# Kernel optimization log

Measured on AMD Instinct MI355X. Metric: run time of the kernel, lower is better.

Reference implementation:

```python
import jax, jax.numpy as jnp
import numpy as np

N = 4096          # num_nodes == batch (every node sampled once)
D_EMB = 512       # n_embd (temporal encoder width)
D_GNN = 256       # gnn_embd
H = 2             # num_heads (hardcoded in GraphAttentionLayer default)
D_HEAD = D_GNN // H
FUS = D_EMB + D_GNN
EDGE_P = 32.0 / N # avg degree ~ max_neighbors
ALPHA = 0.2
NEG_INF = -9e15


def layer_norm(x, g, b, eps=1e-5):
    m = jnp.mean(x, axis=-1, keepdims=True)
    v = jnp.var(x, axis=-1, keepdims=True)
    return (x - m) / jnp.sqrt(v + eps) * g + b


def setup_inputs() -> dict:
    key = jax.random.key(0)
    ks = jax.random.split(key, 12)
    s = lambda fan: 1.0 / np.sqrt(fan)
    h_temporal = jax.random.normal(ks[0], (N, D_EMB), jnp.float32)
    node_indices = jnp.arange(N, dtype=jnp.int32)
    adj = (jax.random.uniform(ks[1], (N, N)) < EDGE_P).astype(jnp.float32)
    adj = jnp.maximum(adj, jnp.eye(N, dtype=jnp.float32))  # self-loops
    W_proj = jax.random.normal(ks[2], (D_EMB, D_GNN), jnp.float32) * s(D_EMB)
    b_proj = jnp.zeros((D_GNN,), jnp.float32)
    W_gat = jax.random.normal(ks[3], (H, D_GNN, D_HEAD), jnp.float32) * s(D_GNN)
    a_gat = jax.random.normal(ks[4], (H, 2 * D_HEAD), jnp.float32) * s(2 * D_HEAD)
    node_emb = jax.random.normal(ks[5], (N, D_GNN), jnp.float32) * 0.02
    ln_g = jnp.ones((D_GNN,), jnp.float32)
    ln_b = jnp.zeros((D_GNN,), jnp.float32)
    ln2_g = jnp.ones((FUS,), jnp.float32)
    ln2_b = jnp.zeros((FUS,), jnp.float32)
    W1 = jax.random.normal(ks[6], (FUS, FUS // 2), jnp.float32) * s(FUS)
    b1 = jnp.zeros((FUS // 2,), jnp.float32)
    W2 = jax.random.normal(ks[7], (FUS // 2, 1), jnp.float32) * s(FUS // 2)
    b2 = jnp.zeros((1,), jnp.float32)
    return dict(h_temporal=h_temporal, node_indices=node_indices, adj=adj,
                W_proj=W_proj, b_proj=b_proj, W_gat=W_gat, a_gat=a_gat,
                node_emb=node_emb, ln_g=ln_g, ln_b=ln_b,
                ln2_g=ln2_g, ln2_b=ln2_b, W1=W1, b1=b1, W2=W2, b2=b2)


def reference(h_temporal, node_indices, adj, W_proj, b_proj, W_gat, a_gat,
              node_emb, ln_g, ln_b, ln2_g, ln2_b, W1, b1, W2, b2):
    # gnn_proj
    h_gnn_in = h_temporal @ W_proj + b_proj                     # (B, D_GNN)
    # scatter-mean of batch features onto graph nodes (torch.unique + index_add_)
    counts = jax.ops.segment_sum(jnp.ones((h_gnn_in.shape[0],), h_gnn_in.dtype),
                                 node_indices, num_segments=N)
    sums = jax.ops.segment_sum(h_gnn_in, node_indices, num_segments=N)
    uniq_feats = sums / jnp.clip(counts, 1.0)[:, None]
    # nodes present in batch use averaged temporal feats, others keep learned embedding
    sub_feats = jnp.where((counts > 0)[:, None], uniq_feats, node_emb)  # (N, D_GNN)
    # multi-head GAT: e[h,i,j] = leakyrelu(a1_h . Wh_i + a2_h . Wh_j)
    Wh = jnp.einsum('ni,hid->hnd', sub_feats, W_gat)            # (H, N, d)
    f_src = jnp.einsum('hnd,hd->hn', Wh, a_gat[:, :D_HEAD])     # query half
    f_dst = jnp.einsum('hnd,hd->hn', Wh, a_gat[:, D_HEAD:])     # key half
    e = jax.nn.leaky_relu(f_src[:, :, None] + f_dst[:, None, :], ALPHA)  # (H,N,N)
    e = jnp.where(adj[None] > 0, e, NEG_INF)
    att = jax.nn.softmax(e, axis=-1)                            # softmax over neighbors j
    hp = jnp.einsum('hnm,hmd->hnd', att, Wh)                    # (H, N, d)
    hp = jnp.transpose(hp, (1, 0, 2)).reshape(N, D_GNN)         # concat heads
    hp = jax.nn.elu(hp)                                         # concat=True
    sub_out = layer_norm(hp, ln_g, ln_b)
    h_graph = sub_out[node_indices]                             # gather back to batch
    # fusion head
    hc = jnp.concatenate([h_temporal, h_graph], axis=-1)        # (B, FUS)
    z = layer_norm(hc, ln2_g, ln2_b)
    z = jax.nn.gelu(z @ W1 + b1, approximate=False)
    out = z @ W2 + b2                                           # (B, 1)
    return out
```

## Files before the change

kernel.cpp:

```cpp
#include <hip/hip_runtime.h>
#include <hip/hip_bf16.h>
#include <math.h>

#define N_NODES 4096
#define D_EMB   512
#define D_GNN   256
#define D_HEAD  128
#define FUS     768
#define D_HID   384
#define MAX_NBR 512

typedef unsigned short u16;
typedef __attribute__((ext_vector_type(4))) float f4;
typedef __attribute__((ext_vector_type(4))) int   i4;
typedef __attribute__((address_space(3))) u16 lds_u16;
typedef __attribute__((address_space(1))) const u16 g_u16;

__device__ __forceinline__ u16 bfh(float x) {
    __hip_bfloat16 b = __float2bfloat16(x);
    return *(u16*)&b;
}
__device__ __forceinline__ float bff(u16 u) {
    __hip_bfloat16 b = *(__hip_bfloat16*)&u;
    return __bfloat162float(b);
}

#define MFMA(acc, a, b) \
    asm volatile("v_mfma_f32_16x16x32_bf16 %0, %1, %2, %0" : "+v"(acc) : "v"(a), "v"(b))

__device__ __forceinline__ float block_reduce(float v, float* red, bool is_max) {
    #pragma unroll
    for (int o = 32; o; o >>= 1)
        v = is_max ? fmaxf(v, __shfl_down(v, o)) : v + __shfl_down(v, o);
    const int wid = threadIdx.x >> 6;
    if ((threadIdx.x & 63) == 0) red[wid] = v;
    __syncthreads();
    float r;
    if (is_max) r = fmaxf(fmaxf(red[0], red[1]), fmaxf(red[2], red[3]));
    else        r = red[0] + red[1] + red[2] + red[3];
    __syncthreads();
    return r;
}

__global__ __launch_bounds__(256) void split_rm(const float* __restrict__ X,
                                                u16* __restrict__ H, u16* __restrict__ L,
                                                int n4) {
    const int i = blockIdx.x * 256 + threadIdx.x;
    if (i >= n4) return;
    const float4 v = ((const float4*)X)[i];
    ushort4 h, l;
    h.x = bfh(v.x); l.x = bfh(v.x - bff(h.x));
    h.y = bfh(v.y); l.y = bfh(v.y - bff(h.y));
    h.z = bfh(v.z); l.z = bfh(v.z - bff(h.z));
    h.w = bfh(v.w); l.w = bfh(v.w - bff(h.w));
    ((ushort4*)H)[i] = h;
    ((ushort4*)L)[i] = l;
}

__device__ __forceinline__ void split_t_body(const float* __restrict__ W,
                                             u16* __restrict__ Th, u16* __restrict__ Tl,
                                             int K, int Nn, int bx, int by,
                                             float (*tile)[33]) {
    const int k0 = by * 32, n0 = bx * 32;
    const int lx = threadIdx.x & 31, ly = threadIdx.x >> 5;
    #pragma unroll
    for (int r = ly; r < 32; r += 8)
        tile[r][lx] = W[(size_t)(k0 + r) * Nn + n0 + lx];
    __syncthreads();
    #pragma unroll
    for (int r = ly; r < 32; r += 8) {
        const float v = tile[lx][r];
        const u16 h = bfh(v);
        const size_t o = (size_t)(n0 + r) * K + k0 + lx;
        Th[o] = h;
        Tl[o] = bfh(v - bff(h));
    }
}

__global__ __launch_bounds__(256) void prep_w(const float* __restrict__ Wproj,
                                              const float* __restrict__ W1,
                                              const float* __restrict__ Wgat,
                                              u16* __restrict__ WpTh, u16* __restrict__ WpTl,
                                              u16* __restrict__ W1Th, u16* __restrict__ W1Tl,
                                              u16* __restrict__ bTh,  u16* __restrict__ bTl) {
    __shared__ float tile[32][33];
    const int b = blockIdx.x;
    if (b < 128) {
        split_t_body(Wproj, WpTh, WpTl, D_EMB, D_GNN, b & 7, b >> 3, tile);
    } else if (b < 416) {
        const int i = b - 128;
        split_t_body(W1, W1Th, W1Tl, FUS, D_HID, i % 12, i / 12, tile);
    } else {
        const int i = b - 416;
        const int n = threadIdx.x;
        const int h = n >> 7, d = n & 127;
        const float v = Wgat[(size_t)h * D_GNN * D_HEAD + (size_t)i * D_HEAD + d];
        const u16 hh = bfh(v);
        bTh[(size_t)n * D_GNN + i] = hh;
        bTl[(size_t)n * D_GNN + i] = bfh(v - bff(hh));
    }
}

template<bool GELU, bool HASB>
__global__ __launch_bounds__(256) void mgemm(const u16* __restrict__ Ah, const u16* __restrict__ Al,
                                             const u16* __restrict__ Bh, const u16* __restrict__ Bl,
                                             const float* __restrict__ bias, float* __restrict__ C,
                                             int M, int Nn, int K) {
    __shared__ u16 lds[3][4][4096];
    const int t = threadIdx.x, w = t >> 6, l = t & 63;
    const int m0 = blockIdx.y * 64, n0 = blockIdx.x * 64;
    const int nk = K >> 6;
    const int r8 = t >> 3;
    const int c8 = (t & 7) ^ (r8 & 7);
    const u16* pAh = Ah + (size_t)(m0 + r8) * K + c8 * 8;
    const u16* pAl = Al + (size_t)(m0 + r8) * K + c8 * 8;
    const u16* pBh = Bh + (size_t)(n0 + r8) * K + c8 * 8;
    const u16* pBl = Bl + (size_t)(n0 + r8) * K + c8 * 8;
    const int w512 = w * 512;
    const int K32 = K * 32;

#define STG(c, koff) do { \
    __builtin_amdgcn_global_load_lds((g_u16*)(pAh + (koff)),       (lds_u16*)&lds[c][0][w512],        16, 0, 0); \
    __builtin_amdgcn_global_load_lds((g_u16*)(pAh + (koff) + K32), (lds_u16*)&lds[c][0][w512 + 2048], 16, 0, 0); \
    __builtin_amdgcn_global_load_lds((g_u16*)(pAl + (koff)),       (lds_u16*)&lds[c][1][w512],        16, 0, 0); \
    __builtin_amdgcn_global_load_lds((g_u16*)(pAl + (koff) + K32), (lds_u16*)&lds[c][1][w512 + 2048], 16, 0, 0); \
    __builtin_amdgcn_global_load_lds((g_u16*)(pBh + (koff)),       (lds_u16*)&lds[c][2][w512],        16, 0, 0); \
    __builtin_amdgcn_global_load_lds((g_u16*)(pBh + (koff) + K32), (lds_u16*)&lds[c][2][w512 + 2048], 16, 0, 0); \
    __builtin_amdgcn_global_load_lds((g_u16*)(pBl + (koff)),       (lds_u16*)&lds[c][3][w512],        16, 0, 0); \
    __builtin_amdgcn_global_load_lds((g_u16*)(pBl + (koff) + K32), (lds_u16*)&lds[c][3][w512 + 2048], 16, 0, 0); \
} while (0)

    const int wm = w >> 1, wn = w & 1;
    const int lr = l & 15;
    const int kq = l >> 4;
    int aoff[2][2], boff[2][2];
    #pragma unroll
    for (int i = 0; i < 2; ++i)
        #pragma unroll
        for (int ks = 0; ks < 2; ++ks) {
            const int ar = wm * 32 + i * 16 + lr;
            const int br = wn * 32 + i * 16 + lr;
            aoff[i][ks] = ar * 64 + (((ks << 2) + kq) ^ (ar & 7)) * 8;
            boff[i][ks] = br * 64 + (((ks << 2) + kq) ^ (br & 7)) * 8;
        }

    f4 acc[2][2] = {};
    STG(0, 0);
    if (nk > 1) STG(1, 64);
    int cur = 0;
    for (int kt = 0; kt < nk; ++kt) {
        const int ahead = nk - 1 - kt;
        if (ahead >= 2) {
            const int nxt2 = (cur >= 1) ? cur - 1 : 2;
            STG(nxt2, (kt + 2) * 64);
            asm volatile("s_waitcnt vmcnt(16)" ::: "memory");
        } else if (ahead == 1) {
            asm volatile("s_waitcnt vmcnt(8)" ::: "memory");
        } else {
            asm volatile("s_waitcnt vmcnt(0)" ::: "memory");
        }
        __builtin_amdgcn_s_barrier();
        __builtin_amdgcn_sched_barrier(0);
        const u16* LAh = lds[cur][0];
        const u16* LAl = lds[cur][1];
        const u16* LBh = lds[cur][2];
        const u16* LBl = lds[cur][3];
        i4 ah[2][2], al_[2][2], bh[2][2], bl_[2][2];
        #pragma unroll
        for (int i = 0; i < 2; ++i)
            #pragma unroll
            for (int ks = 0; ks < 2; ++ks) {
                ah[i][ks]  = *(const i4*)&LAh[aoff[i][ks]];
                al_[i][ks] = *(const i4*)&LAl[aoff[i][ks]];
                bh[i][ks]  = *(const i4*)&LBh[boff[i][ks]];
                bl_[i][ks] = *(const i4*)&LBl[boff[i][ks]];
            }
        #pragma unroll
        for (int i = 0; i < 2; ++i)
            #pragma unroll
            for (int j = 0; j < 2; ++j)
                #pragma unroll
                for (int ks = 0; ks < 2; ++ks) {
                    MFMA(acc[i][j], ah[i][ks],  bh[j][ks]);
                    MFMA(acc[i][j], ah[i][ks],  bl_[j][ks]);
                    MFMA(acc[i][j], al_[i][ks], bh[j][ks]);
                }
        __builtin_amdgcn_sched_barrier(0);
        __builtin_amdgcn_s_barrier();
        cur = (cur == 2) ? 0 : cur + 1;
    }
    asm volatile("s_nop 7\n\ts_nop 7\n\ts_nop 7");
    #pragma unroll
    for (int i = 0; i < 2; ++i)
        #pragma unroll
        for (int j = 0; j < 2; ++j) {
            const int col = n0 + wn * 32 + j * 16 + lr;
            float bv = 0.f;
            if (HASB) bv = bias[col];
            #pragma unroll
            for (int r = 0; r < 4; ++r) {
                const int row = m0 + wm * 32 + i * 16 + (l >> 4) * 4 + r;
                float v = acc[i][j][r] + bv;
                if (GELU) v = 0.5f * v * (1.f + erff(v * 0.70710678118654752f));
                C[(size_t)row * Nn + col] = v;
            }
        }
#undef STG
}

__global__ __launch_bounds__(256) void scatter_add(const float* __restrict__ hgnn,
                                                   const int* __restrict__ nidx,
                                                   float* __restrict__ sums,
                                                   float* __restrict__ counts) {
    const int b = blockIdx.x, t = threadIdx.x;
    const int g = nidx[b];
    atomicAdd(&sums[(size_t)g * D_GNN + t], hgnn[(size_t)b * D_GNN + t]);
    if (t == 0) atomicAdd(&counts[g], 1.0f);
}

__global__ __launch_bounds__(256) void combine(const float* __restrict__ sums,
                                               const float* __restrict__ counts,
                                               const float* __restrict__ nemb,
                                               u16* __restrict__ subh,
                                               u16* __restrict__ subl) {
    const int n = blockIdx.x, t = threadIdx.x;
    const float c = counts[n];
    const size_t o = (size_t)n * D_GNN + t;
    const float v = (c > 0.f) ? sums[o] / fmaxf(c, 1.f) : nemb[o];
    const u16 h = bfh(v);
    subh[o] = h;
    subl[o] = bfh(v - bff(h));
}

__global__ __launch_bounds__(256) void fsd(const float* __restrict__ Wh,
                                           const float* __restrict__ agat,
                                           float* __restrict__ fsrc,
                                           float* __restrict__ fdst) {
    const int n = blockIdx.x * 4 + (threadIdx.x >> 6);
    const int l = threadIdx.x & 63;
    const float* row = Wh + (size_t)n * D_GNN;
    const float x0 = row[l],       x1 = row[l + 64];
    const float y0 = row[128 + l], y1 = row[192 + l];
    float s0 = x0 * agat[l]       + x1 * agat[l + 64];
    float s1 = x0 * agat[128 + l] + x1 * agat[192 + l];
    float s2 = y0 * agat[256 + l] + y1 * agat[320 + l];
    float s3 = y0 * agat[384 + l] + y1 * agat[448 + l];
    #pragma unroll
    for (int o = 32; o; o >>= 1) {
        s0 += __shfl_down(s0, o); s1 += __shfl_down(s1, o);
        s2 += __shfl_down(s2, o); s3 += __shfl_down(s3, o);
    }
    if (l == 0) {
        fsrc[n] = s0;            fdst[n] = s1;
        fsrc[N_NODES + n] = s2;  fdst[N_NODES + n] = s3;
    }
}

__global__ __launch_bounds__(256) void gat_attn(const float* __restrict__ adj,
                                                const float* __restrict__ Wh,
                                                const float* __restrict__ fsrc,
                                                const float* __restrict__ fdst,
                                                const float* __restrict__ lng,
                                                const float* __restrict__ lnb,
                                                float* __restrict__ subout) {
    const int i = blockIdx.x, t = threadIdx.x;
    const int lane = t & 63, wid = t >> 6;
    __shared__ int   s_nbr[MAX_NBR];
    __shared__ int   s_wsum[4];
    __shared__ float s_att[2][MAX_NBR];
    __shared__ float s_red[4];
    __shared__ float s_inv[2];

    const float4* arow4 = (const float4*)(adj + (size_t)i * N_NODES) + t * 4;
    const float4 c0 = arow4[0], c1 = arow4[1], c2 = arow4[2], c3 = arow4[3];
    float v[16];
    *(float4*)&v[0]  = c0; *(float4*)&v[4]  = c1;
    *(float4*)&v[8]  = c2; *(float4*)&v[12] = c3;
    int mask = 0;
    #pragma unroll
    for (int k = 0; k < 16; ++k) mask |= (v[k] > 0.f) ? (1 << k) : 0;
    const int cnt_t = __popc(mask);

    int pre = cnt_t;
    #pragma unroll
    for (int o = 1; o < 64; o <<= 1) {
        const int u = __shfl_up(pre, o);
        if (lane >= o) pre += u;
    }
    if (lane == 63) s_wsum[wid] = pre;
    __syncthreads();
    int base = 0;
    for (int w = 0; w < wid; ++w) base += s_wsum[w];
    const int total = s_wsum[0] + s_wsum[1] + s_wsum[2] + s_wsum[3];
    int off = base + pre - cnt_t;
    #pragma unroll
    for (int k = 0; k < 16; ++k)
        if ((mask >> k) & 1) {
            if (off < MAX_NBR) s_nbr[off] = t * 16 + k;
            ++off;
        }
    __syncthreads();
    const int cnt = min(total, MAX_NBR);

    for (int h = 0; h < 2; ++h) {
        const float fs = fsrc[h * N_NODES + i];
        const float* fd = fdst + h * N_NODES;
        float lm = -1e30f;
        for (int idx = t; idx < cnt; idx += 256) {
            float e = fs + fd[s_nbr[idx]];
            e = e > 0.f ? e : 0.2f * e;
            s_att[h][idx] = e;
            lm = fmaxf(lm, e);
        }
        const float m = block_reduce(lm, s_red, true);
        float ls = 0.f;
        for (int idx = t; idx < cnt; idx += 256) {
            const float p = expf(s_att[h][idx] - m);
            s_att[h][idx] = p;
            ls += p;
        }
        const float s = block_reduce(ls, s_red, false);
        if (t == 0) s_inv[h] = 1.f / s;
    }
    __syncthreads();

    const int h = t >> 7, d = t & 127;
    const float* att = s_att[h];
    const int hd = h * D_HEAD + d;
    float a0 = 0.f, a1 = 0.f, a2 = 0.f, a3 = 0.f;
    int j = 0;
    for (; j + 4 <= cnt; j += 4) {
        a0 += att[j]     * Wh[(size_t)s_nbr[j]     * D_GNN + hd];
        a1 += att[j + 1] * Wh[(size_t)s_nbr[j + 1] * D_GNN + hd];
        a2 += att[j + 2] * Wh[(size_t)s_nbr[j + 2] * D_GNN + hd];
        a3 += att[j + 3] * Wh[(size_t)s_nbr[j + 3] * D_GNN + hd];
    }
    for (; j < cnt; ++j)
        a0 += att[j] * Wh[(size_t)s_nbr[j] * D_GNN + hd];
    float acc = ((a0 + a1) + (a2 + a3)) * s_inv[h];

    const float vv = acc > 0.f ? acc : expm1f(acc);
    const float sum  = block_reduce(vv, s_red, false);
    const float sq   = block_reduce(vv * vv, s_red, false);
    const float mean = sum * (1.f / 256.f);
    const float var  = sq * (1.f / 256.f) - mean * mean;
    const float rstd = rsqrtf(var + 1e-5f);
    subout[(size_t)i * D_GNN + t] = (vv - mean) * rstd * lng[t] + lnb[t];
}

__global__ __launch_bounds__(256) void fuse_ln(const float* __restrict__ ht,
                                               const float* __restrict__ subout,
                                               const int* __restrict__ nidx,
                                               const float* __restrict__ g,
                                               const float* __restrict__ b,
                                               u16* __restrict__ znh,
                                               u16* __restrict__ znl) {
    const int row = blockIdx.x, t = threadIdx.x;
    __shared__ float s_red[4];
    const int gidx = nidx[row];
    const float x0 = ht[(size_t)row * D_EMB + t];
    const float x1 = ht[(size_t)row * D_EMB + 256 + t];
    const float x2 = subout[(size_t)gidx * D_GNN + t];
    const float sum = block_reduce(x0 + x1 + x2, s_red, false);
    const float sq  = block_reduce(x0 * x0 + x1 * x1 + x2 * x2, s_red, false);
    const float mean = sum * (1.f / 768.f);
    const float var  = sq * (1.f / 768.f) - mean * mean;
    const float rstd = rsqrtf(var + 1e-5f);
    const size_t base = (size_t)row * FUS;
    const float z0 = (x0 - mean) * rstd * g[t]       + b[t];
    const float z1 = (x1 - mean) * rstd * g[256 + t] + b[256 + t];
    const float z2 = (x2 - mean) * rstd * g[512 + t] + b[512 + t];
    u16 h;
    h = bfh(z0); znh[base + t]       = h; znl[base + t]       = bfh(z0 - bff(h));
    h = bfh(z1); znh[base + 256 + t] = h; znl[base + 256 + t] = bfh(z1 - bff(h));
    h = bfh(z2); znh[base + 512 + t] = h; znl[base + 512 + t] = bfh(z2 - bff(h));
}

__global__ __launch_bounds__(256) void outk(const float* __restrict__ z1,
                                            const float* __restrict__ W2,
                                            const float* __restrict__ b2,
                                            float* __restrict__ out) {
    const int row = blockIdx.x * 4 + (threadIdx.x >> 6);
    const int l = threadIdx.x & 63;
    float acc = 0.f;
    for (int c = l; c < D_HID; c += 64)
        acc += z1[(size_t)row * D_HID + c] * W2[c];
    #pragma unroll
    for (int o = 32; o; o >>= 1) acc += __shfl_down(acc, o);
    if (l == 0) out[row] = acc + b2[0];
}

extern "C" void kernel_launch(void* const* d_in, const int* in_sizes, int n_in,
                              void* d_out, int out_size, void* d_ws, size_t ws_size,
                              hipStream_t stream) {
    const float* ht    = (const float*)d_in[0];
    const int*   nidx  = (const int*)  d_in[1];
    const float* adj   = (const float*)d_in[2];
    const float* Wproj = (const float*)d_in[3];
    const float* bproj = (const float*)d_in[4];
    const float* Wgat  = (const float*)d_in[5];
    const float* agat  = (const float*)d_in[6];
    const float* nemb  = (const float*)d_in[7];
    const float* lng   = (const float*)d_in[8];
    const float* lnb   = (const float*)d_in[9];
    const float* ln2g  = (const float*)d_in[10];
    const float* ln2b  = (const float*)d_in[11];
    const float* W1    = (const float*)d_in[12];
    const float* b1    = (const float*)d_in[13];
    const float* W2    = (const float*)d_in[14];
    const float* b2    = (const float*)d_in[15];
    float* out = (float*)d_out;

    float* f_sums = (float*)d_ws;
    float* f_cnt  = f_sums + 1048576;
    float* f_hgnn = f_cnt  + 4096;
    float* f_wh   = f_hgnn + 1048576;
    float* f_z1   = f_wh   + 1048576;
    float* f_fsrc = f_z1   + 1572864;
    float* f_fdst = f_fsrc + 8192;
    float* f_subo = f_fdst + 8192;
    u16*   ht_hi  = (u16*)(f_subo + 1048576);
    u16*   ht_lo  = ht_hi  + 2097152;
    u16*   subf_h = ht_lo  + 2097152;
    u16*   subf_l = subf_h + 1048576;
    u16*   zn_hi  = subf_l + 1048576;
    u16*   zn_lo  = zn_hi  + 3145728;
    u16*   WpT_h  = zn_lo  + 3145728;
    u16*   WpT_l  = WpT_h  + 131072;
    u16*   bT_h   = WpT_l  + 131072;
    u16*   bT_l   = bT_h   + 65536;
    u16*   W1T_h  = bT_l   + 65536;
    u16*   W1T_l  = W1T_h  + 294912;

    hipMemsetAsync(f_sums, 0, (1048576 + 4096) * sizeof(float), stream);

    prep_w<<<672, 256, 0, stream>>>(Wproj, W1, Wgat, WpT_h, WpT_l, W1T_h, W1T_l, bT_h, bT_l);
    split_rm<<<2048, 256, 0, stream>>>(ht, ht_hi, ht_lo, 524288);
    mgemm<false, true><<<dim3(4, 64), 256, 0, stream>>>(
        ht_hi, ht_lo, WpT_h, WpT_l, bproj, f_hgnn, N_NODES, D_GNN, D_EMB);
    scatter_add<<<N_NODES, 256, 0, stream>>>(f_hgnn, nidx, f_sums, f_cnt);
    combine<<<N_NODES, 256, 0, stream>>>(f_sums, f_cnt, nemb, subf_h, subf_l);
    mgemm<false, false><<<dim3(4, 64), 256, 0, stream>>>(
        subf_h, subf_l, bT_h, bT_l, nullptr, f_wh, N_NODES, D_GNN, D_GNN);
    fsd<<<N_NODES / 4, 256, 0, stream>>>(f_wh, agat, f_fsrc, f_fdst);
    gat_attn<<<N_NODES, 256, 0, stream>>>(adj, f_wh, f_fsrc, f_fdst, lng, lnb, f_subo);
    fuse_ln<<<N_NODES, 256, 0, stream>>>(ht, f_subo, nidx, ln2g, ln2b, zn_hi, zn_lo);
    mgemm<true, true><<<dim3(6, 64), 256, 0, stream>>>(
        zn_hi, zn_lo, W1T_h, W1T_l, b1, f_z1, N_NODES, D_HID, FUS);
    outk<<<N_NODES / 4, 256, 0, stream>>>(f_z1, W2, b2, out);
}
```

Baseline: 215.1 us.

## Replace async LDS-direct triple buffering with register-staged double buffering; merge prep kernels

The GEMM kernel drops the global_load_lds triple-buffered pipeline and instead loads the next k-tile into registers while computing the current one, then writes it to swizzled LDS with a double buffer and a plain __syncthreads. The MFMA loop is reordered so each k-slice issues hi*hi, hi*lo and lo*hi groups across all four output tiles, which spreads out dependent accumulator updates. The weight prep and activation split kernels are merged into a single launch to save one kernel launch. Register staging raises VGPR use and adds LDS write instructions, and the double buffer allows less latency hiding than the previous three-stage pipeline.

```diff
diff --git a/kernel.cpp b/kernel.cpp
--- a/kernel.cpp
+++ b/kernel.cpp
@@ -13,8 +13,6 @@
 typedef unsigned short u16;
 typedef __attribute__((ext_vector_type(4))) float f4;
 typedef __attribute__((ext_vector_type(4))) int   i4;
-typedef __attribute__((address_space(3))) u16 lds_u16;
-typedef __attribute__((address_space(1))) const u16 g_u16;
 
 __device__ __forceinline__ u16 bfh(float x) {
     __hip_bfloat16 b = __float2bfloat16(x);
@@ -40,21 +38,6 @@
     else        r = red[0] + red[1] + red[2] + red[3];
     __syncthreads();
     return r;
-}
-
-__global__ __launch_bounds__(256) void split_rm(const float* __restrict__ X,
-                                                u16* __restrict__ H, u16* __restrict__ L,
-                                                int n4) {
-    const int i = blockIdx.x * 256 + threadIdx.x;
-    if (i >= n4) return;
-    const float4 v = ((const float4*)X)[i];
-    ushort4 h, l;
-    h.x = bfh(v.x); l.x = bfh(v.x - bff(h.x));
-    h.y = bfh(v.y); l.y = bfh(v.y - bff(h.y));
-    h.z = bfh(v.z); l.z = bfh(v.z - bff(h.z));
-    h.w = bfh(v.w); l.w = bfh(v.w - bff(h.w));
-    ((ushort4*)H)[i] = h;
-    ((ushort4*)L)[i] = l;
 }
 
 __device__ __forceinline__ void split_t_body(const float* __restrict__ W,
@@ -77,12 +60,14 @@
     }
 }
 
-__global__ __launch_bounds__(256) void prep_w(const float* __restrict__ Wproj,
-                                              const float* __restrict__ W1,
-                                              const float* __restrict__ Wgat,
-                                              u16* __restrict__ WpTh, u16* __restrict__ WpTl,
-                                              u16* __restrict__ W1Th, u16* __restrict__ W1Tl,
-                                              u16* __restrict__ bTh,  u16* __restrict__ bTl) {
+__global__ __launch_bounds__(256) void prep_all(const float* __restrict__ Wproj,
+                                                const float* __restrict__ W1,
+                                                const float* __restrict__ Wgat,
+                                                const float* __restrict__ ht,
+                                                u16* __restrict__ WpTh, u16* __restrict__ WpTl,
+                                                u16* __restrict__ W1Th, u16* __restrict__ W1Tl,
+                                                u16* __restrict__ bTh,  u16* __restrict__ bTl,
+                                                u16* __restrict__ htH,  u16* __restrict__ htL) {
     __shared__ float tile[32][33];
     const int b = blockIdx.x;
     if (b < 128) {
@@ -90,7 +75,7 @@
     } else if (b < 416) {
         const int i = b - 128;
         split_t_body(W1, W1Th, W1Tl, FUS, D_HID, i % 12, i / 12, tile);
-    } else {
+    } else if (b < 672) {
         const int i = b - 416;
         const int n = threadIdx.x;
         const int h = n >> 7, d = n & 127;
@@ -98,6 +83,16 @@
         const u16 hh = bfh(v);
         bTh[(size_t)n * D_GNN + i] = hh;
         bTl[(size_t)n * D_GNN + i] = bfh(v - bff(hh));
+    } else {
+        const int i = (b - 672) * 256 + threadIdx.x;
+        const float4 v = ((const float4*)ht)[i];
+        ushort4 h, l;
+        h.x = bfh(v.x); l.x = bfh(v.x - bff(h.x));
+        h.y = bfh(v.y); l.y = bfh(v.y - bff(h.y));
+        h.z = bfh(v.z); l.z = bfh(v.z - bff(h.z));
+        h.w = bfh(v.w); l.w = bfh(v.w - bff(h.w));
+        ((ushort4*)htH)[i] = h;
+        ((ushort4*)htL)[i] = l;
     }
 }
 
@@ -106,28 +101,32 @@
                                              const u16* __restrict__ Bh, const u16* __restrict__ Bl,
                                              const float* __restrict__ bias, float* __restrict__ C,
                                              int M, int Nn, int K) {
-    __shared__ u16 lds[3][4][4096];
+    __shared__ u16 lds[2][4][4096];
     const int t = threadIdx.x, w = t >> 6, l = t & 63;
     const int m0 = blockIdx.y * 64, n0 = blockIdx.x * 64;
     const int nk = K >> 6;
     const int r8 = t >> 3;
-    const int c8 = (t & 7) ^ (r8 & 7);
+    const int c8 = t & 7;
     const u16* pAh = Ah + (size_t)(m0 + r8) * K + c8 * 8;
     const u16* pAl = Al + (size_t)(m0 + r8) * K + c8 * 8;
     const u16* pBh = Bh + (size_t)(n0 + r8) * K + c8 * 8;
     const u16* pBl = Bl + (size_t)(n0 + r8) * K + c8 * 8;
-    const int w512 = w * 512;
     const int K32 = K * 32;
-
-#define STG(c, koff) do { \
-    __builtin_amdgcn_global_load_lds((g_u16*)(pAh + (koff)),       (lds_u16*)&lds[c][0][w512],        16, 0, 0); \
-    __builtin_amdgcn_global_load_lds((g_u16*)(pAh + (koff) + K32), (lds_u16*)&lds[c][0][w512 + 2048], 16, 0, 0); \
-    __builtin_amdgcn_global_load_lds((g_u16*)(pAl + (koff)),       (lds_u16*)&lds[c][1][w512],        16, 0, 0); \
-    __builtin_amdgcn_global_load_lds((g_u16*)(pAl + (koff) + K32), (lds_u16*)&lds[c][1][w512 + 2048], 16, 0, 0); \
-    __builtin_amdgcn_global_load_lds((g_u16*)(pBh + (koff)),       (lds_u16*)&lds[c][2][w512],        16, 0, 0); \
-    __builtin_amdgcn_global_load_lds((g_u16*)(pBh + (koff) + K32), (lds_u16*)&lds[c][2][w512 + 2048], 16, 0, 0); \
-    __builtin_amdgcn_global_load_lds((g_u16*)(pBl + (koff)),       (lds_u16*)&lds[c][3][w512],        16, 0, 0); \
-    __builtin_amdgcn_global_load_lds((g_u16*)(pBl + (koff) + K32), (lds_u16*)&lds[c][3][w512 + 2048], 16, 0, 0); \
+    const int wr0 = r8 * 64 + (c8 ^ (r8 & 7)) * 8;
+    const int wr1 = wr0 + 2048;
+
+    i4 rAh0, rAh1, rAl0, rAl1, rBh0, rBh1, rBl0, rBl1;
+#define LOADR(koff) do { \
+    rAh0 = *(const i4*)(pAh + (koff)); rAh1 = *(const i4*)(pAh + (koff) + K32); \
+    rAl0 = *(const i4*)(pAl + (koff)); rAl1 = *(const i4*)(pAl + (koff) + K32); \
+    rBh0 = *(const i4*)(pBh + (koff)); rBh1 = *(const i4*)(pBh + (koff) + K32); \
+    rBl0 = *(const i4*)(pBl + (koff)); rBl1 = *(const i4*)(pBl + (koff) + K32); \
+} while (0)
+#define WRITEL(c) do { \
+    *(i4*)&lds[c][0][wr0] = rAh0; *(i4*)&lds[c][0][wr1] = rAh1; \
+    *(i4*)&lds[c][1][wr0] = rAl0; *(i4*)&lds[c][1][wr1] = rAl1; \
+    *(i4*)&lds[c][2][wr0] = rBh0; *(i4*)&lds[c][2][wr1] = rBh1; \
+    *(i4*)&lds[c][3][wr0] = rBl0; *(i4*)&lds[c][3][wr1] = rBl1; \
 } while (0)
 
     const int wm = w >> 1, wn = w & 1;
@@ -145,22 +144,12 @@
         }
 
     f4 acc[2][2] = {};
-    STG(0, 0);
-    if (nk > 1) STG(1, 64);
+    LOADR(0);
+    WRITEL(0);
+    __syncthreads();
     int cur = 0;
     for (int kt = 0; kt < nk; ++kt) {
-        const int ahead = nk - 1 - kt;
-        if (ahead >= 2) {
-            const int nxt2 = (cur >= 1) ? cur - 1 : 2;
-            STG(nxt2, (kt + 2) * 64);
-            asm volatile("s_waitcnt vmcnt(16)" ::: "memory");
-        } else if (ahead == 1) {
-            asm volatile("s_waitcnt vmcnt(8)" ::: "memory");
-        } else {
-            asm volatile("s_waitcnt vmcnt(0)" ::: "memory");
-        }
-        __builtin_amdgcn_s_barrier();
-        __builtin_amdgcn_sched_barrier(0);
+        if (kt + 1 < nk) LOADR((kt + 1) * 64);
         const u16* LAh = lds[cur][0];
         const u16* LAl = lds[cur][1];
         const u16* LBh = lds[cur][2];
@@ -176,18 +165,26 @@
                 bl_[i][ks] = *(const i4*)&LBl[boff[i][ks]];
             }
         #pragma unroll
-        for (int i = 0; i < 2; ++i)
+        for (int ks = 0; ks < 2; ++ks) {
             #pragma unroll
-            for (int j = 0; j < 2; ++j)
+            for (int i = 0; i < 2; ++i)
                 #pragma unroll
-                for (int ks = 0; ks < 2; ++ks) {
-                    MFMA(acc[i][j], ah[i][ks],  bh[j][ks]);
-                    MFMA(acc[i][j], ah[i][ks],  bl_[j][ks]);
+                for (int j = 0; j < 2; ++j)
+                    MFMA(acc[i][j], ah[i][ks], bh[j][ks]);
+            #pragma unroll
+            for (int i = 0; i < 2; ++i)
+                #pragma unroll
+                for (int j = 0; j < 2; ++j)
+                    MFMA(acc[i][j], ah[i][ks], bl_[j][ks]);
+            #pragma unroll
+            for (int i = 0; i < 2; ++i)
+                #pragma unroll
+                for (int j = 0; j < 2; ++j)
                     MFMA(acc[i][j], al_[i][ks], bh[j][ks]);
-                }
-        __builtin_amdgcn_sched_barrier(0);
-        __builtin_amdgcn_s_barrier();
-        cur = (cur == 2) ? 0 : cur + 1;
+        }
+        if (kt + 1 < nk) WRITEL(cur ^ 1);
+        __syncthreads();
+        cur ^= 1;
     }
     asm volatile("s_nop 7\n\ts_nop 7\n\ts_nop 7");
     #pragma unroll
@@ -205,7 +202,8 @@
                 C[(size_t)row * Nn + col] = v;
             }
         }
-#undef STG
+#undef LOADR
+#undef WRITEL
 }
 
 __global__ __launch_bounds__(256) void scatter_add(const float* __restrict__ hgnn,
@@ -434,8 +432,9 @@
 
     hipMemsetAsync(f_sums, 0, (1048576 + 4096) * sizeof(float), stream);
 
-    prep_w<<<672, 256, 0, stream>>>(Wproj, W1, Wgat, WpT_h, WpT_l, W1T_h, W1T_l, bT_h, bT_l);
-    split_rm<<<2048, 256, 0, stream>>>(ht, ht_hi, ht_lo, 524288);
+    prep_all<<<2720, 256, 0, stream>>>(Wproj, W1, Wgat, ht,
+                                       WpT_h, WpT_l, W1T_h, W1T_l, bT_h, bT_l,
+                                       ht_hi, ht_lo);
     mgemm<false, true><<<dim3(4, 64), 256, 0, stream>>>(
         ht_hi, ht_lo, WpT_h, WpT_l, bproj, f_hgnn, N_NODES, D_GNN, D_EMB);
     scatter_add<<<N_NODES, 256, 0, stream>>>(f_hgnn, nidx, f_sums, f_cnt);
```

After: 207.4 us. 1.04x faster.
